# Optimization experiments

Measured on AMD Instinct MI355X. Metric: run time of the kernel, lower is better.

Reference implementation:

```python
import jax, jax.numpy as jnp
import numpy as np

B, S, D = 2, 2048, 1024
H, DK, DV = 16, 64, 64
DFF = 4096
EPS_RMS = 1e-6


def setup_inputs() -> dict:
    key = jax.random.key(0)
    ks = jax.random.split(key, 10)
    sc = 0.02
    return {
        "x": jax.random.normal(ks[0], (B, S, D), jnp.float32),
        "w_q": jax.random.normal(ks[1], (D, H * DK), jnp.float32) * sc,
        "w_k": jax.random.normal(ks[2], (D, H * DK), jnp.float32) * sc,
        "w_v": jax.random.normal(ks[3], (D, H * DV), jnp.float32) * sc,
        "w_o": jax.random.normal(ks[4], (H * DV, D), jnp.float32) * sc,
        "w_gate": jax.random.normal(ks[5], (D, DFF), jnp.float32) * sc,
        "w_up": jax.random.normal(ks[6], (D, DFF), jnp.float32) * sc,
        "w_down": jax.random.normal(ks[7], (DFF, D), jnp.float32) * sc,
        "g1": jnp.ones((D,), jnp.float32),
        "g2": jnp.ones((D,), jnp.float32),
    }


def _rmsnorm(x, g):
    var = jnp.mean(jnp.square(x), axis=-1, keepdims=True)
    return x * jax.lax.rsqrt(var + EPS_RMS) * g


def _stable_softmax(s):
    # Faithful to source: exp(x) / (sum exp(x) + 1e-9); fully-masked rows -> 0.
    e = jnp.exp(s)
    return e / (jnp.sum(e, axis=-1, keepdims=True) + 1e-9)


def reference(x, w_q, w_k, w_v, w_o, w_gate, w_up, w_down, g1, g2):
    b, s, d = x.shape
    h = _rmsnorm(x, g1)
    q = (h @ w_q).reshape(b, s, H, DK).transpose(0, 2, 1, 3)  # [B,H,S,DK]
    k = (h @ w_k).reshape(b, s, H, DK).transpose(0, 2, 1, 3)
    v = (h @ w_v).reshape(b, s, H, DV).transpose(0, 2, 1, 3)
    scores = jnp.einsum("bhqd,bhkd->bhqk", q, k) / jnp.sqrt(jnp.asarray(DK, x.dtype))
    # triu with diagonal=0: self and future positions are masked
    mask = jnp.triu(jnp.ones((s, s), bool))
    scores = jnp.where(mask, -jnp.inf, scores)
    attn = _stable_softmax(scores)  # [B,H,S,S]
    av = jnp.einsum("bhqk,bhkd->bhqd", attn, v)
    av = av.transpose(0, 2, 1, 3).reshape(b, s, H * DV)
    x = x + av @ w_o  # residual 1
    h2 = _rmsnorm(x, g2)
    hidden = jax.nn.silu(h2 @ w_gate) * (h2 @ w_up)
    return x + hidden @ w_down  # residual 2
```

## Files before the change

### kernel.cpp

```cpp
#include <hip/hip_runtime.h>
#include <cstdint>
#include <cstddef>

typedef unsigned short u16;
typedef unsigned char u8;
typedef unsigned int u32;
typedef __bf16 bf16x8 __attribute__((ext_vector_type(8)));
typedef float floatx4 __attribute__((ext_vector_type(4)));
typedef float floatx16 __attribute__((ext_vector_type(16)));
typedef int i32x8 __attribute__((ext_vector_type(8)));

#define B_ 2
#define S_ 2048
#define D_ 1024
#define H_ 16
#define DFF_ 4096
#define BS_ 4096

__device__ __forceinline__ u16 f2bf(float f) {
  u32 u = __builtin_bit_cast(u32, f);
  u += 0x7fffu + ((u >> 16) & 1u);
  return (u16)(u >> 16);
}
__device__ __forceinline__ float bf2f(u16 h) {
  u32 u = ((u32)h) << 16;
  return __builtin_bit_cast(float, u);
}

__device__ __forceinline__ u32 cvtpk_bf16(float lo, float hi) {
  u32 r;
  asm("v_cvt_pk_bf16_f32 %0, %1, %2" : "=v"(r) : "v"(lo), "v"(hi));
  return r;
}

__device__ __forceinline__ float fexp2(float x) {
  float r;
  asm("v_exp_f32 %0, %1" : "=v"(r) : "v"(x));
  return r;
}

__device__ __forceinline__ u32 f2e4m3(float f) {
  u32 u = __builtin_bit_cast(u32, f);
  const u32 s = (u >> 24) & 0x80u;
  const u32 au = u & 0x7fffffffu;
  if (au < 0x3c800000u) return s;
  if (au > 0x43e00000u) return s | 0x7eu;
  const u32 lsb = (au >> 20) & 1u;
  const u32 r = au + 0x0007ffffu + lsb;
  const u32 e = (r >> 23) & 0xffu;
  const u32 m = (r >> 20) & 7u;
  return s | (((e - 120u) & 0xfu) << 3) | m;
}

__device__ __forceinline__ void gl_lds16(const void* g, void* l) {
  __builtin_amdgcn_global_load_lds(
      (const __attribute__((address_space(1))) void*)g,
      (__attribute__((address_space(3))) void*)l, 16, 0, 0);
}

__device__ __forceinline__ void xcd_swz(int GX, int GY, int& bx, int& by) {
  int flat = by * GX + bx;
  const int q = (GX * GY) >> 3;
  flat = (flat & 7) * q + (flat >> 3);
  bx = flat % GX;
  by = flat / GX;
}

__global__ void prep_weights(const float* __restrict__ wq, const float* __restrict__ wk,
                             const float* __restrict__ wv, const float* __restrict__ wo,
                             const float* __restrict__ wg, const float* __restrict__ wu,
                             const float* __restrict__ wd,
                             u16* __restrict__ wqkv_t, u16* __restrict__ wo_t,
                             u8* __restrict__ wguf8, u16* __restrict__ wdn_t) {
  __shared__ float tile[32][33];
  const int id = blockIdx.x;
  const float* src;
  u16* dst = nullptr;
  int R, C, bx, by, mode;
  if (id < 3072) {
    const int which = id >> 10, lo = id & 1023;
    src = which == 0 ? wq : (which == 1 ? wk : wv);
    dst = wqkv_t + which * 1024 * 1024;
    R = 1024; C = 1024; bx = lo & 31; by = lo >> 5; mode = 0;
  } else if (id < 4096) {
    const int lo = id - 3072;
    src = wo; dst = wo_t; R = 1024; C = 1024; bx = lo & 31; by = lo >> 5; mode = 0;
  } else if (id < 8192) {
    const int lo = id - 4096;
    src = wg; R = 1024; C = 4096; bx = lo & 127; by = lo >> 7; mode = 1;
  } else if (id < 12288) {
    const int lo = id - 8192;
    src = wu; R = 1024; C = 4096; bx = lo & 127; by = lo >> 7; mode = 2;
  } else {
    const int lo = id - 12288;
    src = wd; dst = wdn_t; R = 4096; C = 1024; bx = lo & 31; by = lo >> 5; mode = 0;
  }
  const int tx = threadIdx.x, ty = threadIdx.y;
  const int c0 = bx * 32, r0 = by * 32;
#pragma unroll
  for (int i = 0; i < 4; i++)
    tile[ty + i * 8][tx] = src[(size_t)(r0 + ty + i * 8) * C + c0 + tx];
  __syncthreads();
  const int sx = ty * 32 + tx;
  const int oci = sx >> 3, cg = (sx & 7) * 4;
  const int oc = c0 + oci;
  const float v0 = tile[cg][oci], v1 = tile[cg + 1][oci];
  const float v2 = tile[cg + 2][oci], v3 = tile[cg + 3][oci];
  if (mode == 0) {
    uint2 o;
    o.x = (u32)f2bf(v0) | ((u32)f2bf(v1) << 16);
    o.y = (u32)f2bf(v2) | ((u32)f2bf(v3) << 16);
    *(uint2*)(dst + (size_t)oc * R + r0 + cg) = o;
  } else {
    const int orow = (oc >> 5) * 64 + (oc & 31) + (mode == 2 ? 32 : 0);
    const u32 p = f2e4m3(v0 * 64.f) | (f2e4m3(v1 * 64.f) << 8) |
                  (f2e4m3(v2 * 64.f) << 16) | (f2e4m3(v3 * 64.f) << 24);
    *(u32*)(wguf8 + (size_t)orow * 1024 + r0 + cg) = p;
  }
}

template <int F8>
__global__ __launch_bounds__(256) void rmsnorm_kernel(const float* __restrict__ x,
                                                      const float* __restrict__ g,
                                                      void* __restrict__ out) {
  const int row = blockIdx.x, t = threadIdx.x;
  const float4 v = ((const float4*)(x + (size_t)row * 1024))[t];
  float ss = v.x * v.x + v.y * v.y + v.z * v.z + v.w * v.w;
#pragma unroll
  for (int off = 32; off > 0; off >>= 1) ss += __shfl_xor(ss, off);
  __shared__ float red[4];
  if ((t & 63) == 0) red[t >> 6] = ss;
  __syncthreads();
  ss = red[0] + red[1] + red[2] + red[3];
  const float inv = rsqrtf(ss * (1.0f / 1024.0f) + 1e-6f);
  const float4 gv = ((const float4*)g)[t];
  const float y0 = v.x * inv * gv.x, y1 = v.y * inv * gv.y;
  const float y2 = v.z * inv * gv.z, y3 = v.w * inv * gv.w;
  if (F8) {
    const u32 p = f2e4m3(y0) | (f2e4m3(y1) << 8) | (f2e4m3(y2) << 16) | (f2e4m3(y3) << 24);
    ((u32*)out)[(size_t)row * 256 + t] = p;
  } else {
    uint2 o;
    o.x = (u32)f2bf(y0) | ((u32)f2bf(y1) << 16);
    o.y = (u32)f2bf(y2) | ((u32)f2bf(y3) << 16);
    ((uint2*)out)[(size_t)row * 256 + t] = o;
  }
}

template <int BN>
__device__ __forceinline__ void bt_step(const u16* Asb, const u16* Bsb,
                                        floatx16 (&acc)[2][BN / 64],
                                        int wm, int wn, int c31, int khalf) {
  constexpr int NTI = BN / 64;
#pragma unroll
  for (int ks = 0; ks < 4; ks++) {
    bf16x8 af[2], bfr[NTI];
#pragma unroll
    for (int mi = 0; mi < 2; mi++) {
      const int row = wm * 64 + mi * 32 + c31;
      const int e = (ks * 2 + khalf) ^ (row & 7);
      af[mi] = *(const bf16x8*)(Asb + row * 64 + e * 8);
    }
#pragma unroll
    for (int ni = 0; ni < NTI; ni++) {
      const int row = wn * (BN / 2) + ni * 32 + c31;
      const int e = (ks * 2 + khalf) ^ (row & 7);
      bfr[ni] = *(const bf16x8*)(Bsb + row * 64 + e * 8);
    }
#pragma unroll
    for (int mi = 0; mi < 2; mi++)
#pragma unroll
      for (int ni = 0; ni < NTI; ni++)
        acc[mi][ni] = __builtin_amdgcn_mfma_f32_32x32x16_bf16(af[mi], bfr[ni],
                                                              acc[mi][ni], 0, 0, 0);
  }
}

template <int BN, int EPI, int PIPE>
__global__ __launch_bounds__(256) void gemm_bt(const u16* __restrict__ A,
                                               const u16* __restrict__ Bt,
                                               void* __restrict__ Cout,
                                               const float* __restrict__ res,
                                               u16* __restrict__ vTout,
                                               int M, int N, int K) {
  constexpr int NBUF = PIPE ? 2 : 1;
  __shared__ u16 As[NBUF][128 * 64];
  __shared__ u16 Bs[NBUF][BN * 64];
  constexpr int NTI = BN / 64;
  constexpr int NSEG = 16 + BN / 8;
  constexpr int SPW = NSEG / 4;
  const int t = threadIdx.x, w = t >> 6, l = t & 63;

  int bx = (int)blockIdx.x, by = (int)blockIdx.y;
  xcd_swz((int)gridDim.x, (int)gridDim.y, bx, by);
  const int m0 = by * 128, n0 = bx * BN;
  const int wm = w >> 1, wn = w & 1;
  const int c31 = l & 31, khalf = l >> 5;

  const u16* gsrc[SPW];
  u16* ld0[SPW];
  u16* ld1[SPW];
  {
    const int rl = l >> 3, ch = (l & 7) ^ rl;
#pragma unroll
    for (int i = 0; i < SPW; i++) {
      const int s = w * SPW + i;
      if (s < 16) {
        gsrc[i] = A + (size_t)(m0 + s * 8 + rl) * K + ch * 8;
        ld0[i] = As[0] + s * 512;
        ld1[i] = As[NBUF - 1] + s * 512;
      } else {
        gsrc[i] = Bt + (size_t)(n0 + (s - 16) * 8 + rl) * K + ch * 8;
        ld0[i] = Bs[0] + (s - 16) * 512;
        ld1[i] = Bs[NBUF - 1] + (s - 16) * 512;
      }
    }
  }

  floatx16 acc[2][NTI] = {};

  if constexpr (!PIPE) {
    for (int kk = 0; kk < K; kk += 64) {
      __syncthreads();
#pragma unroll
      for (int i = 0; i < SPW; i++) gl_lds16(gsrc[i], ld0[i]);
#pragma unroll
      for (int i = 0; i < SPW; i++) gsrc[i] += 64;
      __syncthreads();
      bt_step<BN>(As[0], Bs[0], acc, wm, wn, c31, khalf);
    }
  } else {
#pragma unroll
    for (int i = 0; i < SPW; i++) gl_lds16(gsrc[i], ld0[i]);
#pragma unroll
    for (int i = 0; i < SPW; i++) gsrc[i] += 64;
    asm volatile("s_waitcnt vmcnt(0)" ::: "memory");
    __builtin_amdgcn_s_barrier();
    for (int kk = 0; kk < K; kk += 128) {
#pragma unroll
      for (int i = 0; i < SPW; i++) gl_lds16(gsrc[i], ld1[i]);
#pragma unroll
      for (int i = 0; i < SPW; i++) gsrc[i] += 64;
      bt_step<BN>(As[0], Bs[0], acc, wm, wn, c31, khalf);
      asm volatile("s_waitcnt vmcnt(0)" ::: "memory");
      __builtin_amdgcn_s_barrier();
      if (kk + 128 < K) {
#pragma unroll
        for (int i = 0; i < SPW; i++) gl_lds16(gsrc[i], ld0[i]);
#pragma unroll
        for (int i = 0; i < SPW; i++) gsrc[i] += 64;
      }
      bt_step<BN>(As[NBUF - 1], Bs[NBUF - 1], acc, wm, wn, c31, khalf);
      asm volatile("s_waitcnt vmcnt(0)" ::: "memory");
      __builtin_amdgcn_s_barrier();
    }
  }

  if constexpr (EPI == 3) {
    if (n0 >= 2048) {
#pragma unroll
      for (int mi = 0; mi < 2; mi++)
#pragma unroll
        for (int ni = 0; ni < NTI; ni++) {
          const int col = n0 + wn * (BN / 2) + ni * 32 + c31 - 2048;
          const int hh = col >> 6, dv = col & 63;
          const int rbase = m0 + wm * 64 + mi * 32 + 4 * khalf;
          const int bb = rbase >> 11;
          u16* vp = vTout + (size_t)((bb * 16 + hh) * 64 + dv) * 2048 + (rbase & 2047);
#pragma unroll
          for (int rg = 0; rg < 4; rg++) {
            uint2 pk;
            pk.x = (u32)f2bf(acc[mi][ni][rg * 4 + 0]) |
                   ((u32)f2bf(acc[mi][ni][rg * 4 + 1]) << 16);
            pk.y = (u32)f2bf(acc[mi][ni][rg * 4 + 2]) |
                   ((u32)f2bf(acc[mi][ni][rg * 4 + 3]) << 16);
            *(uint2*)(vp + rg * 8) = pk;
          }
        }
      return;
    }
  }
#pragma unroll
  for (int mi = 0; mi < 2; mi++)
#pragma unroll
    for (int ni = 0; ni < NTI; ni++) {
      const int col = n0 + wn * (BN / 2) + ni * 32 + c31;
#pragma unroll
      for (int reg = 0; reg < 16; reg++) {
        const int row = m0 + wm * 64 + mi * 32 + (reg & 3) + 8 * (reg >> 2) + 4 * khalf;
        const size_t idx = (size_t)row * N + col;
        if (EPI == 1) ((float*)Cout)[idx] = acc[mi][ni][reg] + res[idx];
        else          ((u16*)Cout)[idx] = f2bf(acc[mi][ni][reg]);
      }
    }
}

__device__ __forceinline__ void f8_step(const u8* Asb, const u8* Bsb,
                                        floatx16 (&acc)[2][2],
                                        int wm, int wn, int c31, int hf) {
  i32x8 af[2], bf[2];
#pragma unroll
  for (int mi = 0; mi < 2; mi++) {
    const int r = wm * 64 + mi * 32 + c31;
    const int g = (r >> 1) & 3;
    const uint4 lo = *(const uint4*)(Asb + r * 64 + ((2 * hf) ^ g) * 16);
    const uint4 hi = *(const uint4*)(Asb + r * 64 + ((2 * hf + 1) ^ g) * 16);
    af[mi] = i32x8{(int)lo.x, (int)lo.y, (int)lo.z, (int)lo.w,
                   (int)hi.x, (int)hi.y, (int)hi.z, (int)hi.w};
  }
#pragma unroll
  for (int ni = 0; ni < 2; ni++) {
    const int r = wn * 64 + ni * 32 + c31;
    const int g = (r >> 1) & 3;
    const uint4 lo = *(const uint4*)(Bsb + r * 64 + ((2 * hf) ^ g) * 16);
    const uint4 hi = *(const uint4*)(Bsb + r * 64 + ((2 * hf + 1) ^ g) * 16);
    bf[ni] = i32x8{(int)lo.x, (int)lo.y, (int)lo.z, (int)lo.w,
                   (int)hi.x, (int)hi.y, (int)hi.z, (int)hi.w};
  }
#pragma unroll
  for (int mi = 0; mi < 2; mi++)
#pragma unroll
    for (int ni = 0; ni < 2; ni++)
      acc[mi][ni] = __builtin_amdgcn_mfma_scale_f32_32x32x64_f8f6f4(
          af[mi], bf[ni], acc[mi][ni], 0, 0,
          0, 0x7F7F7F7F,
          0, 0x79797979);
}

__global__ __launch_bounds__(256) void gemm_f8(const u8* __restrict__ A,
                                               const u8* __restrict__ B,
                                               u16* __restrict__ hid,
                                               int M, int K) {
  __shared__ u8 As[2][128 * 64];
  __shared__ u8 Bs[2][128 * 64];
  const int t = threadIdx.x, w = t >> 6, l = t & 63;
  int bx = (int)blockIdx.x, by = (int)blockIdx.y;
  xcd_swz((int)gridDim.x, (int)gridDim.y, bx, by);
  const int m0 = by * 128, n0 = bx * 128;
  const int wm = w >> 1, wn = w & 1;
  const int c31 = l & 31, hf = l >> 5;

  const u8* gsrc[4];
  u8* ld0[4];
  u8* ld1[4];
  {
    const int rl = l >> 2, ch = (l & 3) ^ ((l >> 3) & 3);
#pragma unroll
    for (int i = 0; i < 4; i++) {
      const int s = w * 4 + i;
      if (s < 8) {
        gsrc[i] = A + (size_t)(m0 + s * 16 + rl) * K + ch * 16;
        ld0[i] = As[0] + s * 1024;
        ld1[i] = As[1] + s * 1024;
      } else {
        gsrc[i] = B + (size_t)(n0 + (s - 8) * 16 + rl) * K + ch * 16;
        ld0[i] = Bs[0] + (s - 8) * 1024;
        ld1[i] = Bs[1] + (s - 8) * 1024;
      }
    }
  }

  floatx16 acc[2][2] = {};

#pragma unroll
  for (int i = 0; i < 4; i++) gl_lds16(gsrc[i], ld0[i]);
  asm volatile("s_waitcnt vmcnt(0)" ::: "memory");
  __builtin_amdgcn_s_barrier();
  for (int kk = 0; kk < K; kk += 128) {
#pragma unroll
    for (int i = 0; i < 4; i++) gl_lds16(gsrc[i] + kk + 64, ld1[i]);
    f8_step(As[0], Bs[0], acc, wm, wn, c31, hf);
    asm volatile("s_waitcnt vmcnt(0)" ::: "memory");
    __builtin_amdgcn_s_barrier();
    if (kk + 128 < K) {
#pragma unroll
      for (int i = 0; i < 4; i++) gl_lds16(gsrc[i] + kk + 128, ld0[i]);
    }
    f8_step(As[1], Bs[1], acc, wm, wn, c31, hf);
    asm volatile("s_waitcnt vmcnt(0)" ::: "memory");
    __builtin_amdgcn_s_barrier();
  }

#pragma unroll
  for (int mi = 0; mi < 2; mi++) {
    const int colo = (bx * 2 + wn) * 32 + c31;
#pragma unroll
    for (int reg = 0; reg < 16; reg++) {
      const int row = m0 + wm * 64 + mi * 32 + (reg & 3) + 8 * (reg >> 2) + 4 * hf;
      const float g = acc[mi][0][reg];
      const float u = acc[mi][1][reg];
      hid[(size_t)row * 4096 + colo] = f2bf(g / (1.f + __expf(-g)) * u);
    }
  }
}

__global__ __launch_bounds__(256) void attn_kernel(const u16* __restrict__ qkv,
                                                   const u16* __restrict__ vT,
                                                   u16* __restrict__ av) {
  __shared__ u16 SM[2 * 8192];
  __shared__ u16 Ps[4 * 2048];
  const int t = threadIdx.x, w = t >> 6, l = t & 63;
  const int lrow = l & 15, lk = l >> 4;
  const int bh = blockIdx.x;
  const int b = bh >> 4, h = bh & 15;
  const int qt = 15 - (int)blockIdx.y;
  const int qbase = qt * 128 + w * 32;
  const int ktmax = 2 * qt + 1;
  u16* Pw = Ps + w * 2048;
  const float SC = 0.125f * 1.44269504088896f;

  bf16x8 aq[2][2];
#pragma unroll
  for (int sub = 0; sub < 2; sub++)
#pragma unroll
    for (int half = 0; half < 2; half++)
      aq[sub][half] = *(const bf16x8*)(qkv + (size_t)(b * S_ + qbase + sub * 16 + lrow) * 3072 +
                                       h * 64 + half * 32 + lk * 8);

  const u16* gcur[4];
  int gstep[4], loff[4];
#pragma unroll
  for (int i = 0; i < 4; i++) {
    const int c = w + 4 * i;
    const int half = (c >> 2) & 1, grp = c & 3;
    if (c < 8) {
      gcur[i] = qkv + (size_t)(b * S_ + grp * 16 + (l >> 2)) * 3072 + D_ + h * 64 +
                half * 32 + (l & 3) * 8;
      gstep[i] = 64 * 3072;
      loff[i] = half * 2048 + grp * 512;
    } else {
      gcur[i] = vT + (size_t)(bh * 64 + grp * 16 + (l >> 2)) * S_ + half * 32 + (l & 3) * 8;
      gstep[i] = 64;
      loff[i] = 4096 + half * 2048 + grp * 512;
    }
  }

  floatx4 oacc[2][4] = {};
  float den[2] = {0.f, 0.f};

  int cur = 0;
#pragma unroll
  for (int i = 0; i < 4; i++) { gl_lds16(gcur[i], SM + loff[i]); gcur[i] += gstep[i]; }

  for (int kt = 0; kt <= ktmax; kt++) {
    __syncthreads();
    if (kt < ktmax) {
#pragma unroll
      for (int i = 0; i < 4; i++) {
        gl_lds16(gcur[i], SM + (cur ^ 1) * 8192 + loff[i]);
        gcur[i] += gstep[i];
      }
    }
    const u16* Kbuf = SM + cur * 8192;
    const u16* Vbuf = Kbuf + 4096;

    const bool active = (kt * 64 < qbase + 31);
    if (active) {
      const bool need_mask = (kt * 64 + 64 > qbase);

      bf16x8 bk[4][2];
#pragma unroll
      for (int ct = 0; ct < 4; ct++)
#pragma unroll
        for (int half = 0; half < 2; half++)
          bk[ct][half] = *(const bf16x8*)(Kbuf + half * 2048 + (ct * 16 + lrow) * 32 + lk * 8);

      floatx4 sf[2][4] = {};
      __builtin_amdgcn_s_setprio(1);
#pragma unroll
      for (int sub = 0; sub < 2; sub++)
#pragma unroll
        for (int ct = 0; ct < 4; ct++) {
          sf[sub][ct] = __builtin_amdgcn_mfma_f32_16x16x32_bf16(bk[ct][0], aq[sub][0],
                                                                sf[sub][ct], 0, 0, 0);
          sf[sub][ct] = __builtin_amdgcn_mfma_f32_16x16x32_bf16(bk[ct][1], aq[sub][1],
                                                                sf[sub][ct], 0, 0, 0);
        }
      __builtin_amdgcn_s_setprio(0);

      if (!need_mask) {
#pragma unroll
        for (int sub = 0; sub < 2; sub++) {
          const int prow = sub * 16 + lrow;
#pragma unroll
          for (int ct = 0; ct < 4; ct++) {
            const float p0 = fexp2(sf[sub][ct][0] * SC);
            const float p1 = fexp2(sf[sub][ct][1] * SC);
            const float p2 = fexp2(sf[sub][ct][2] * SC);
            const float p3 = fexp2(sf[sub][ct][3] * SC);
            den[sub] += (p0 + p1) + (p2 + p3);
            uint2 pk;
            pk.x = cvtpk_bf16(p0, p1);
            pk.y = cvtpk_bf16(p2, p3);
            *(uint2*)(Pw + prow * 64 + (((2 * ct + (lk >> 1)) ^ (lrow & 7)) << 3) +
                      (lk & 1) * 4) = pk;
          }
        }
      } else {
#pragma unroll
        for (int sub = 0; sub < 2; sub++) {
          const int qp = qbase + sub * 16 + lrow;
          const int prow = sub * 16 + lrow;
#pragma unroll
          for (int ct = 0; ct < 4; ct++) {
            const int kb = kt * 64 + ct * 16 + lk * 4;
            const float p0 = (kb + 0 < qp) ? fexp2(sf[sub][ct][0] * SC) : 0.f;
            const float p1 = (kb + 1 < qp) ? fexp2(sf[sub][ct][1] * SC) : 0.f;
            const float p2 = (kb + 2 < qp) ? fexp2(sf[sub][ct][2] * SC) : 0.f;
            const float p3 = (kb + 3 < qp) ? fexp2(sf[sub][ct][3] * SC) : 0.f;
            den[sub] += (p0 + p1) + (p2 + p3);
            uint2 pk;
            pk.x = cvtpk_bf16(p0, p1);
            pk.y = cvtpk_bf16(p2, p3);
            *(uint2*)(Pw + prow * 64 + (((2 * ct + (lk >> 1)) ^ (lrow & 7)) << 3) +
                      (lk & 1) * 4) = pk;
          }
        }
      }

      bf16x8 ap[2][2], bv[4][2];
#pragma unroll
      for (int sub = 0; sub < 2; sub++)
#pragma unroll
        for (int kh = 0; kh < 2; kh++) {
          const int prow = sub * 16 + lrow;
          ap[sub][kh] = *(const bf16x8*)(Pw + prow * 64 + (((kh * 4 + lk) ^ (prow & 7)) << 3));
        }
#pragma unroll
      for (int ni = 0; ni < 4; ni++)
#pragma unroll
        for (int kh = 0; kh < 2; kh++)
          bv[ni][kh] = *(const bf16x8*)(Vbuf + kh * 2048 + (ni * 16 + lrow) * 32 + lk * 8);
      __builtin_amdgcn_s_setprio(1);
#pragma unroll
      for (int sub = 0; sub < 2; sub++)
#pragma unroll
        for (int ni = 0; ni < 4; ni++) {
          oacc[sub][ni] = __builtin_amdgcn_mfma_f32_16x16x32_bf16(ap[sub][0], bv[ni][0],
                                                                  oacc[sub][ni], 0, 0, 0);
          oacc[sub][ni] = __builtin_amdgcn_mfma_f32_16x16x32_bf16(ap[sub][1], bv[ni][1],
                                                                  oacc[sub][ni], 0, 0, 0);
        }
      __builtin_amdgcn_s_setprio(0);
    }
    cur ^= 1;
  }

#pragma unroll
  for (int sub = 0; sub < 2; sub++) {
    den[sub] += __shfl_xor(den[sub], 16);
    den[sub] += __shfl_xor(den[sub], 32);
  }
  float dq[2][4];
#pragma unroll
  for (int sub = 0; sub < 2; sub++)
#pragma unroll
    for (int r = 0; r < 4; r++)
      dq[sub][r] = __shfl(den[sub], lk * 4 + r);

#pragma unroll
  for (int sub = 0; sub < 2; sub++)
#pragma unroll
    for (int ni = 0; ni < 4; ni++)
#pragma unroll
      for (int r = 0; r < 4; r++) {
        const int row = qbase + sub * 16 + lk * 4 + r;
        const int col = h * 64 + ni * 16 + lrow;
        av[(size_t)(b * S_ + row) * 1024 + col] = f2bf(oacc[sub][ni][r] / (dq[sub][r] + 1e-9f));
      }
}

#define OFF_WQKV 0u
#define OFF_WO   6291456u
#define OFF_WGU8 8388608u
#define OFF_WDN  16777216u
#define OFF_H1   25165824u
#define OFF_QKV  33554432u
#define OFF_VT   58720256u
#define OFF_AV   67108864u
#define OFF_X1   75497472u
#define OFF_H2F8 92274688u
#define OFF_HID  96468992u

extern "C" void kernel_launch(void* const* d_in, const int* in_sizes, int n_in,
                              void* d_out, int out_size, void* d_ws, size_t ws_size,
                              hipStream_t stream) {
  const float* x      = (const float*)d_in[0];
  const float* w_q    = (const float*)d_in[1];
  const float* w_k    = (const float*)d_in[2];
  const float* w_v    = (const float*)d_in[3];
  const float* w_o    = (const float*)d_in[4];
  const float* w_gate = (const float*)d_in[5];
  const float* w_up   = (const float*)d_in[6];
  const float* w_down = (const float*)d_in[7];
  const float* g1     = (const float*)d_in[8];
  const float* g2     = (const float*)d_in[9];

  char* ws = (char*)d_ws;
  u16* wqkv_t = (u16*)(ws + OFF_WQKV);
  u16* wo_t   = (u16*)(ws + OFF_WO);
  u8*  wguf8  = (u8*)(ws + OFF_WGU8);
  u16* wdn_t  = (u16*)(ws + OFF_WDN);
  u16* h1     = (u16*)(ws + OFF_H1);
  u16* qkv    = (u16*)(ws + OFF_QKV);
  u16* vT     = (u16*)(ws + OFF_VT);
  u16* av     = (u16*)(ws + OFF_AV);
  float* x1   = (float*)(ws + OFF_X1);
  u8*  h2f8   = (u8*)(ws + OFF_H2F8);
  u16* hid    = (u16*)(ws + OFF_HID);
  float* out  = (float*)d_out;

  prep_weights<<<16384, dim3(32, 8), 0, stream>>>(w_q, w_k, w_v, w_o, w_gate, w_up, w_down,
                                                  wqkv_t, wo_t, wguf8, wdn_t);

  rmsnorm_kernel<0><<<BS_, 256, 0, stream>>>(x, g1, h1);
  gemm_bt<64, 3, 1><<<dim3(3072 / 64, BS_ / 128), 256, 0, stream>>>(
      h1, wqkv_t, qkv, nullptr, vT, BS_, 3072, 1024);
  attn_kernel<<<dim3(32, 16), 256, 0, stream>>>(qkv, vT, av);
  gemm_bt<64, 1, 1><<<dim3(1024 / 64, BS_ / 128), 256, 0, stream>>>(
      av, wo_t, x1, x, nullptr, BS_, 1024, 1024);
  rmsnorm_kernel<1><<<BS_, 256, 0, stream>>>(x1, g2, h2f8);
  gemm_f8<<<dim3(4096 / 64, BS_ / 128), 256, 0, stream>>>(h2f8, wguf8, hid, BS_, 1024);
  gemm_bt<64, 1, 1><<<dim3(1024 / 64, BS_ / 128), 256, 0, stream>>>(
      hid, wdn_t, out, x1, nullptr, BS_, 1024, 4096);
}
```

Before: 344.5 us.

## Triple-buffer GEMM K-loop with partial vmcnt waits and raise MFMA priority

The bf16 and fp8 GEMM kernels move from a double-buffered loop that drains all loads (vmcnt(0)) every step to a three-stage LDS ring. Each step waits only for the oldest outstanding tile and keeps the next tile's global-to-LDS loads in flight, which should hide more memory latency behind MFMA work. The MFMA blocks are also wrapped in s_setprio so waves doing math are favoured by the scheduler. The cost is 1.5x the LDS per block, which may lower occupancy. The hard-coded vmcnt literals tie the code to a fixed number of loads per wave, guarded by a static_assert in the bf16 kernel.

```diff
diff --git a/kernel.cpp b/kernel.cpp
--- a/kernel.cpp
+++ b/kernel.cpp
@@ -65,6 +65,8 @@
   bx = flat % GX;
   by = flat / GX;
 }
+
+#define WAITB(N) asm volatile("s_waitcnt vmcnt(" #N ")\n\ts_barrier" ::: "memory")
 
 __global__ void prep_weights(const float* __restrict__ wq, const float* __restrict__ wk,
                              const float* __restrict__ wv, const float* __restrict__ wo,
@@ -167,28 +169,41 @@
       const int e = (ks * 2 + khalf) ^ (row & 7);
       bfr[ni] = *(const bf16x8*)(Bsb + row * 64 + e * 8);
     }
+    __builtin_amdgcn_s_setprio(1);
 #pragma unroll
     for (int mi = 0; mi < 2; mi++)
 #pragma unroll
       for (int ni = 0; ni < NTI; ni++)
         acc[mi][ni] = __builtin_amdgcn_mfma_f32_32x32x16_bf16(af[mi], bfr[ni],
                                                               acc[mi][ni], 0, 0, 0);
-  }
-}
-
-template <int BN, int EPI, int PIPE>
+    __builtin_amdgcn_s_setprio(0);
+  }
+}
+
+template <int SPW>
+__device__ __forceinline__ void bt_issue(const u16* (&gsrc)[SPW], u16* const (&ld0)[SPW],
+                                         int bufofs) {
+#pragma unroll
+  for (int i = 0; i < SPW; i++) gl_lds16(gsrc[i], ld0[i] + bufofs);
+#pragma unroll
+  for (int i = 0; i < SPW; i++) gsrc[i] += 64;
+}
+
+template <int BN, int EPI>
 __global__ __launch_bounds__(256) void gemm_bt(const u16* __restrict__ A,
                                                const u16* __restrict__ Bt,
                                                void* __restrict__ Cout,
                                                const float* __restrict__ res,
                                                u16* __restrict__ vTout,
                                                int M, int N, int K) {
-  constexpr int NBUF = PIPE ? 2 : 1;
-  __shared__ u16 As[NBUF][128 * 64];
-  __shared__ u16 Bs[NBUF][BN * 64];
   constexpr int NTI = BN / 64;
+  constexpr int ASZ = 128 * 64;
+  constexpr int BSZ = BN * 64;
+  constexpr int STRIDE = ASZ + BSZ;
+  __shared__ u16 SMEM[3 * STRIDE];
   constexpr int NSEG = 16 + BN / 8;
   constexpr int SPW = NSEG / 4;
+  static_assert(SPW == 6, "vmcnt literal assumes 6 loads/wave/tile");
   const int t = threadIdx.x, w = t >> 6, l = t & 63;
 
   int bx = (int)blockIdx.x, by = (int)blockIdx.y;
@@ -199,7 +214,6 @@
 
   const u16* gsrc[SPW];
   u16* ld0[SPW];
-  u16* ld1[SPW];
   {
     const int rl = l >> 3, ch = (l & 7) ^ rl;
 #pragma unroll
@@ -207,54 +221,32 @@
       const int s = w * SPW + i;
       if (s < 16) {
         gsrc[i] = A + (size_t)(m0 + s * 8 + rl) * K + ch * 8;
-        ld0[i] = As[0] + s * 512;
-        ld1[i] = As[NBUF - 1] + s * 512;
+        ld0[i] = SMEM + s * 512;
       } else {
         gsrc[i] = Bt + (size_t)(n0 + (s - 16) * 8 + rl) * K + ch * 8;
-        ld0[i] = Bs[0] + (s - 16) * 512;
-        ld1[i] = Bs[NBUF - 1] + (s - 16) * 512;
+        ld0[i] = SMEM + ASZ + (s - 16) * 512;
       }
     }
   }
 
   floatx16 acc[2][NTI] = {};
 
-  if constexpr (!PIPE) {
-    for (int kk = 0; kk < K; kk += 64) {
-      __syncthreads();
-#pragma unroll
-      for (int i = 0; i < SPW; i++) gl_lds16(gsrc[i], ld0[i]);
-#pragma unroll
-      for (int i = 0; i < SPW; i++) gsrc[i] += 64;
-      __syncthreads();
-      bt_step<BN>(As[0], Bs[0], acc, wm, wn, c31, khalf);
-    }
-  } else {
-#pragma unroll
-    for (int i = 0; i < SPW; i++) gl_lds16(gsrc[i], ld0[i]);
-#pragma unroll
-    for (int i = 0; i < SPW; i++) gsrc[i] += 64;
-    asm volatile("s_waitcnt vmcnt(0)" ::: "memory");
-    __builtin_amdgcn_s_barrier();
-    for (int kk = 0; kk < K; kk += 128) {
-#pragma unroll
-      for (int i = 0; i < SPW; i++) gl_lds16(gsrc[i], ld1[i]);
-#pragma unroll
-      for (int i = 0; i < SPW; i++) gsrc[i] += 64;
-      bt_step<BN>(As[0], Bs[0], acc, wm, wn, c31, khalf);
-      asm volatile("s_waitcnt vmcnt(0)" ::: "memory");
-      __builtin_amdgcn_s_barrier();
-      if (kk + 128 < K) {
-#pragma unroll
-        for (int i = 0; i < SPW; i++) gl_lds16(gsrc[i], ld0[i]);
-#pragma unroll
-        for (int i = 0; i < SPW; i++) gsrc[i] += 64;
-      }
-      bt_step<BN>(As[NBUF - 1], Bs[NBUF - 1], acc, wm, wn, c31, khalf);
-      asm volatile("s_waitcnt vmcnt(0)" ::: "memory");
-      __builtin_amdgcn_s_barrier();
-    }
-  }
+#define BT_STEP(CB) bt_step<BN>(SMEM + (CB)*STRIDE, SMEM + (CB)*STRIDE + ASZ, \
+                                acc, wm, wn, c31, khalf)
+
+  bt_issue<SPW>(gsrc, ld0, 0 * STRIDE);
+  bt_issue<SPW>(gsrc, ld0, 1 * STRIDE);
+  const int NT = K >> 6;
+  for (int rep = 0; rep < (NT - 4) / 3; rep++) {
+    WAITB(6); bt_issue<SPW>(gsrc, ld0, 2 * STRIDE); BT_STEP(0);
+    WAITB(6); bt_issue<SPW>(gsrc, ld0, 0 * STRIDE); BT_STEP(1);
+    WAITB(6); bt_issue<SPW>(gsrc, ld0, 1 * STRIDE); BT_STEP(2);
+  }
+  WAITB(6); bt_issue<SPW>(gsrc, ld0, 2 * STRIDE); BT_STEP(0);
+  WAITB(6); bt_issue<SPW>(gsrc, ld0, 0 * STRIDE); BT_STEP(1);
+  WAITB(6); BT_STEP(2);
+  WAITB(0); BT_STEP(0);
+#undef BT_STEP
 
   if constexpr (EPI == 3) {
     if (n0 >= 2048) {
@@ -317,6 +309,7 @@
     bf[ni] = i32x8{(int)lo.x, (int)lo.y, (int)lo.z, (int)lo.w,
                    (int)hi.x, (int)hi.y, (int)hi.z, (int)hi.w};
   }
+  __builtin_amdgcn_s_setprio(1);
 #pragma unroll
   for (int mi = 0; mi < 2; mi++)
 #pragma unroll
@@ -325,14 +318,23 @@
           af[mi], bf[ni], acc[mi][ni], 0, 0,
           0, 0x7F7F7F7F,
           0, 0x79797979);
+  __builtin_amdgcn_s_setprio(0);
+}
+
+__device__ __forceinline__ void f8_issue(const u8* (&gsrc)[4], u8* const (&ld0)[4],
+                                         int bufofs) {
+#pragma unroll
+  for (int i = 0; i < 4; i++) gl_lds16(gsrc[i], ld0[i] + bufofs);
+#pragma unroll
+  for (int i = 0; i < 4; i++) gsrc[i] += 64;
 }
 
 __global__ __launch_bounds__(256) void gemm_f8(const u8* __restrict__ A,
                                                const u8* __restrict__ B,
                                                u16* __restrict__ hid,
                                                int M, int K) {
-  __shared__ u8 As[2][128 * 64];
-  __shared__ u8 Bs[2][128 * 64];
+  constexpr int STRIDE = 2 * 128 * 64;
+  __shared__ u8 SMEM[3 * STRIDE];
   const int t = threadIdx.x, w = t >> 6, l = t & 63;
   int bx = (int)blockIdx.x, by = (int)blockIdx.y;
   xcd_swz((int)gridDim.x, (int)gridDim.y, bx, by);
@@ -342,7 +344,6 @@
 
   const u8* gsrc[4];
   u8* ld0[4];
-  u8* ld1[4];
   {
     const int rl = l >> 2, ch = (l & 3) ^ ((l >> 3) & 3);
 #pragma unroll
@@ -350,36 +351,32 @@
       const int s = w * 4 + i;
       if (s < 8) {
         gsrc[i] = A + (size_t)(m0 + s * 16 + rl) * K + ch * 16;
-        ld0[i] = As[0] + s * 1024;
-        ld1[i] = As[1] + s * 1024;
+        ld0[i] = SMEM + s * 1024;
       } else {
         gsrc[i] = B + (size_t)(n0 + (s - 8) * 16 + rl) * K + ch * 16;
-        ld0[i] = Bs[0] + (s - 8) * 1024;
-        ld1[i] = Bs[1] + (s - 8) * 1024;
+        ld0[i] = SMEM + 8192 + (s - 8) * 1024;
       }
     }
   }
 
   floatx16 acc[2][2] = {};
 
-#pragma unroll
-  for (int i = 0; i < 4; i++) gl_lds16(gsrc[i], ld0[i]);
-  asm volatile("s_waitcnt vmcnt(0)" ::: "memory");
-  __builtin_amdgcn_s_barrier();
-  for (int kk = 0; kk < K; kk += 128) {
-#pragma unroll
-    for (int i = 0; i < 4; i++) gl_lds16(gsrc[i] + kk + 64, ld1[i]);
-    f8_step(As[0], Bs[0], acc, wm, wn, c31, hf);
-    asm volatile("s_waitcnt vmcnt(0)" ::: "memory");
-    __builtin_amdgcn_s_barrier();
-    if (kk + 128 < K) {
-#pragma unroll
-      for (int i = 0; i < 4; i++) gl_lds16(gsrc[i] + kk + 128, ld0[i]);
-    }
-    f8_step(As[1], Bs[1], acc, wm, wn, c31, hf);
-    asm volatile("s_waitcnt vmcnt(0)" ::: "memory");
-    __builtin_amdgcn_s_barrier();
-  }
+#define F8_STEP(CB) f8_step(SMEM + (CB)*STRIDE, SMEM + (CB)*STRIDE + 8192, \
+                            acc, wm, wn, c31, hf)
+
+  f8_issue(gsrc, ld0, 0 * STRIDE);
+  f8_issue(gsrc, ld0, 1 * STRIDE);
+  const int NT = K >> 6;
+  for (int rep = 0; rep < (NT - 4) / 3; rep++) {
+    WAITB(4); f8_issue(gsrc, ld0, 2 * STRIDE); F8_STEP(0);
+    WAITB(4); f8_issue(gsrc, ld0, 0 * STRIDE); F8_STEP(1);
+    WAITB(4); f8_issue(gsrc, ld0, 1 * STRIDE); F8_STEP(2);
+  }
+  WAITB(4); f8_issue(gsrc, ld0, 2 * STRIDE); F8_STEP(0);
+  WAITB(4); f8_issue(gsrc, ld0, 0 * STRIDE); F8_STEP(1);
+  WAITB(4); F8_STEP(2);
+  WAITB(0); F8_STEP(0);
+#undef F8_STEP
 
 #pragma unroll
   for (int mi = 0; mi < 2; mi++) {
@@ -614,13 +611,13 @@
                                                   wqkv_t, wo_t, wguf8, wdn_t);
 
   rmsnorm_kernel<0><<<BS_, 256, 0, stream>>>(x, g1, h1);
-  gemm_bt<64, 3, 1><<<dim3(3072 / 64, BS_ / 128), 256, 0, stream>>>(
+  gemm_bt<64, 3><<<dim3(3072 / 64, BS_ / 128), 256, 0, stream>>>(
       h1, wqkv_t, qkv, nullptr, vT, BS_, 3072, 1024);
   attn_kernel<<<dim3(32, 16), 256, 0, stream>>>(qkv, vT, av);
-  gemm_bt<64, 1, 1><<<dim3(1024 / 64, BS_ / 128), 256, 0, stream>>>(
+  gemm_bt<64, 1><<<dim3(1024 / 64, BS_ / 128), 256, 0, stream>>>(
       av, wo_t, x1, x, nullptr, BS_, 1024, 1024);
   rmsnorm_kernel<1><<<BS_, 256, 0, stream>>>(x1, g2, h2f8);
   gemm_f8<<<dim3(4096 / 64, BS_ / 128), 256, 0, stream>>>(h2f8, wguf8, hid, BS_, 1024);
-  gemm_bt<64, 1, 1><<<dim3(1024 / 64, BS_ / 128), 256, 0, stream>>>(
+  gemm_bt<64, 1><<<dim3(1024 / 64, BS_ / 128), 256, 0, stream>>>(
       hid, wdn_t, out, x1, nullptr, BS_, 1024, 4096);
 }
```

New measurement: 348.2 us. Within noise of the previous version (+1.1%).
